# Optimization experiments

Measured on AMD Instinct MI355X. Metric: run time of the kernel, lower is better.

## Reference

```python
import jax, jax.numpy as jnp
import numpy as np

ALPHA = 0.15
KSIZE = 5
EPS = 1e-6


def _minmax_norm(x):
    # x: [B,1,H,W]; per-sample min-max normalize, 0.5 if nearly constant
    mn = x.min(axis=(1, 2, 3), keepdims=True)
    mx = x.max(axis=(1, 2, 3), keepdims=True)
    denom = mx - mn
    safe = jnp.where(denom > EPS, denom, 1.0)
    return jnp.where(denom > EPS, (x - mn) / safe, 0.5)


def _saliency_map(images, out_hw):
    # grayscale via luma weights
    w = jnp.array([0.299, 0.587, 0.114], dtype=images.dtype).reshape(1, 3, 1, 1)
    gray = (images * w).sum(axis=1, keepdims=True)  # [B,1,H,W]
    kernel = jnp.ones((1, 1, KSIZE, KSIZE), dtype=gray.dtype) / (KSIZE * KSIZE)
    dn = ('NCHW', 'OIHW', 'NCHW')
    local_mean = jax.lax.conv_general_dilated(gray, kernel, (1, 1), 'SAME', dimension_numbers=dn)
    local_mean_sq = jax.lax.conv_general_dilated(gray ** 2, kernel, (1, 1), 'SAME', dimension_numbers=dn)
    local_var = jnp.maximum(local_mean_sq - local_mean ** 2, 0.0)
    sal = _minmax_norm(local_var)
    if sal.shape[-2:] != out_hw:
        sal = jax.image.resize(sal, (sal.shape[0], 1, out_hw[0], out_hw[1]), method='bilinear')
    return jax.lax.stop_gradient(sal)  # computed under no_grad / detached in torch


def setup_inputs() -> dict:
    key = jax.random.key(0)
    k1, k2 = jax.random.split(key)
    features = jax.random.normal(k1, (64, 512, 28, 28), dtype=jnp.float32)
    images = jax.random.uniform(k2, (64, 3, 224, 224), dtype=jnp.float32)
    return {"features": features, "images": images}


def reference(features, images):
    sal = _saliency_map(images, features.shape[-2:])  # [B,1,Hf,Wf]
    attn = jnp.sqrt((features ** 2).mean(axis=1, keepdims=True))  # [B,1,Hf,Wf]
    attn = _minmax_norm(attn)
    loss = jnp.mean((attn - sal) ** 2)
    return ALPHA * loss
```

## Files before the change

### kernel.cpp

```cpp
#include <hip/hip_runtime.h>
#include <math.h>

#define BATCH 64
#define HIMG 224
#define WIMG 224
#define IMGPLANE (HIMG*WIMG)
#define CF 512
#define HF 28
#define WF 28
#define POS (HF*WF)
#define ALPHA_C 0.15f
#define EPS_C 1e-6f

#define STRIPS 14
#define SROWS 16
#define GROWS 20
#define GCOLS 228
#define GSTR 229
#define VSTR 261

#define NATTN 512
#define NVARH (STRIPS*BATCH)

#define OFF_HRES 0
#define HRES_CNT (BATCH*HIMG*WF)
#define OFF_BMM (OFF_HRES + HRES_CNT)
#define OFF_AP  (OFF_BMM + BATCH*STRIPS*2)
#define OFF_ACC (OFF_AP + 2*BATCH*POS)
#define OFF_CNT (OFF_ACC + 1)

__global__ __launch_bounds__(256) void fat_k(const float* __restrict__ img,
                                             const float* __restrict__ f,
                                             float* __restrict__ ws) {
    __shared__ float g[GROWS * GSTR];
    __shared__ float v[SROWS * VSTR];
    __shared__ float wred[8];
    int bid = blockIdx.x;
    int tid = threadIdx.x;

    if (bid < NATTN) {
        if (bid == 0 && tid == 0) {
            ws[OFF_ACC] = 0.0f;
            ((unsigned*)ws)[OFF_CNT] = 0u;
        }
        int p = (bid & 3) * 256 + tid;
        int b = (bid >> 2) & 63, z = bid >> 8;
        if (p >= POS) return;
        const float* fp = f + ((size_t)b * CF + (size_t)z * 256) * POS + p;
        float acc = 0.0f;
        #pragma unroll 16
        for (int c = 0; c < 256; c++) {
            float u = fp[(size_t)c * POS];
            acc += u * u;
        }
        ws[OFF_AP + ((size_t)z * BATCH + b) * POS + p] = acc;
        return;
    }

    int vb = bid - NATTN;
    int b = vb / STRIPS, sy = vb - b * STRIPS;
    int y0 = sy * SROWS;
    const float* imb = img + (size_t)b * 3 * IMGPLANE;

    for (int i = tid; i < GROWS * GCOLS; i += 256) {
        int gr = i / GCOLS, gc = i - gr * GCOLS;
        int gy = y0 - 2 + gr, gx = gc - 2;
        float u = 0.0f;
        if ((unsigned)gy < HIMG && (unsigned)gx < WIMG) {
            int o = gy * WIMG + gx;
            u = 0.299f * imb[o] + 0.587f * imb[IMGPLANE + o] + 0.114f * imb[2 * IMGPLANE + o];
        }
        g[gr * GSTR + gc] = u;
    }
    if (tid < SROWS * 8) {
        int r = tid >> 3, p = tid & 7;
        int jh = p + ((p < 4) ? 0 : 224);
        v[r * VSTR + jh + (jh >> 3)] = 0.0f;
    }
    __syncthreads();

    int r = tid >> 4, s = tid & 15;
    int x0 = 14 * s;
    const float* gr0 = g + r * GSTR;
    float c1[5], c2[5];
    #pragma unroll
    for (int m = 0; m < 5; m++) {
        float a = 0.0f, a2 = 0.0f;
        #pragma unroll
        for (int k = 0; k < 5; k++) {
            float u = gr0[k * GSTR + x0 + m];
            a += u; a2 += u * u;
        }
        c1[m] = a; c2[m] = a2;
    }
    float vmn = INFINITY, vmx = 0.0f;
    #pragma unroll
    for (int xi = 0; xi < 14; xi++) {
        int p = xi % 5;
        float s1 = c1[p], s2 = c2[p];
        #pragma unroll
        for (int m = 1; m < 5; m++) {
            s1 += c1[(p + m) % 5];
            s2 += c2[(p + m) % 5];
        }
        float m1 = s1 * 0.04f, m2 = s2 * 0.04f;
        float vv = fmaxf(m2 - m1 * m1, 0.0f);
        int jh = x0 + xi + 4;
        v[r * VSTR + jh + (jh >> 3)] = vv;
        vmn = fminf(vmn, vv); vmx = fmaxf(vmx, vv);
        if (xi < 13) {
            float a = 0.0f, a2 = 0.0f;
            #pragma unroll
            for (int k = 0; k < 5; k++) {
                float u = gr0[k * GSTR + x0 + xi + 5];
                a += u; a2 += u * u;
            }
            c1[p] = a; c2[p] = a2;
        }
    }
    #pragma unroll
    for (int o = 32; o > 0; o >>= 1) {
        vmn = fminf(vmn, __shfl_xor(vmn, o));
        vmx = fmaxf(vmx, __shfl_xor(vmx, o));
    }
    int w = tid >> 6;
    if ((tid & 63) == 0) { wred[w] = vmn; wred[4 + w] = vmx; }
    __syncthreads();
    if (tid == 0) {
        float mn = fminf(fminf(wred[0], wred[1]), fminf(wred[2], wred[3]));
        float mx = fmaxf(fmaxf(wred[4], wred[5]), fmaxf(wred[6], wred[7]));
        int blk = b * STRIPS + sy;
        ws[OFF_BMM + 2 * blk]     = mn;
        ws[OFF_BMM + 2 * blk + 1] = mx;
    }

    float* hb = ws + OFF_HRES + ((size_t)b * HIMG + y0) * WF;
    for (int idx = tid; idx < SROWS * WF; idx += 256) {
        int rr = idx / WF, i = idx - rr * WF;
        float acc = 0.0f, wsum = 0.0f;
        int j0 = 8 * i - 4;
        #pragma unroll
        for (int t = 0; t < 16; t++) {
            int j = j0 + t;
            float w_ = 8.0f - fabsf((float)t - 7.5f);
            int jh = j + 4;
            acc += w_ * v[rr * VSTR + jh + (jh >> 3)];
            if ((unsigned)j < WIMG) wsum += w_;
        }
        hb[idx] = acc / wsum;
    }
}

__global__ __launch_bounds__(256) void fused_k(float* __restrict__ ws,
                                               float* __restrict__ out) {
    __shared__ float hres[HIMG][WF + 1];
    __shared__ float wred[4];
    __shared__ float s_mn, s_mx;
    int b = blockIdx.x;
    int tid = threadIdx.x;

    if (tid < 64) {
        float mn = INFINITY, mx = 0.0f;
        if (tid < STRIPS) {
            mn = ws[OFF_BMM + 2 * (b * STRIPS + tid)];
            mx = ws[OFF_BMM + 2 * (b * STRIPS + tid) + 1];
        }
        #pragma unroll
        for (int o = 8; o > 0; o >>= 1) {
            mn = fminf(mn, __shfl_down(mn, o));
            mx = fmaxf(mx, __shfl_down(mx, o));
        }
        if (tid == 0) { s_mn = mn; s_mx = mx; }
    }

    const float* hg = ws + OFF_HRES + (size_t)b * HIMG * WF;
    for (int i = tid; i < HIMG * WF; i += 256) {
        int y = i / WF, x = i - y * WF;
        hres[y][x] = hg[i];
    }
    __syncthreads();

    float vmn = s_mn, vmx = s_mx;
    float vden = vmx - vmn;
    bool vok = vden > EPS_C;

    const float* a0 = ws + OFF_AP + (size_t)b * POS;
    const float* a1 = ws + OFF_AP + ((size_t)BATCH + b) * POS;
    float salv[4], attnv[4];
    float amn = INFINITY, amx = -INFINITY;
    #pragma unroll
    for (int k = 0; k < 4; k++) {
        int idx = tid + 256 * k;
        salv[k] = 0.0f; attnv[k] = 0.0f;
        if (idx < POS) {
            int yo = idx / WF, x = idx - yo * WF;
            float acc = 0.0f, wsum = 0.0f;
            int j0 = 8 * yo - 4;
            #pragma unroll
            for (int t = 0; t < 16; t++) {
                int j = j0 + t;
                float w = 8.0f - fabsf((float)t - 7.5f);
                if ((unsigned)j < HIMG) { acc += w * hres[j][x]; wsum += w; }
            }
            float sraw = acc / wsum;
            salv[k] = vok ? (sraw - vmn) / vden : 0.5f;
            float a = sqrtf((a0[idx] + a1[idx]) * (1.0f / CF));
            attnv[k] = a;
            amn = fminf(amn, a); amx = fmaxf(amx, a);
        }
    }

    #pragma unroll
    for (int o = 32; o > 0; o >>= 1) {
        amn = fminf(amn, __shfl_xor(amn, o));
        amx = fmaxf(amx, __shfl_xor(amx, o));
    }
    int w = tid >> 6;
    if ((tid & 63) == 0) wred[w] = amn;
    __syncthreads();
    if (tid == 0) s_mn = fminf(fminf(wred[0], wred[1]), fminf(wred[2], wred[3]));
    __syncthreads();
    if ((tid & 63) == 0) wred[w] = amx;
    __syncthreads();
    if (tid == 0) s_mx = fmaxf(fmaxf(wred[0], wred[1]), fmaxf(wred[2], wred[3]));
    __syncthreads();
    amn = s_mn; amx = s_mx;
    float aden = amx - amn;
    bool aok = aden > EPS_C;

    float lsum = 0.0f;
    #pragma unroll
    for (int k = 0; k < 4; k++) {
        int idx = tid + 256 * k;
        if (idx < POS) {
            float an = aok ? (attnv[k] - amn) / aden : 0.5f;
            float d = an - salv[k];
            lsum += d * d;
        }
    }
    #pragma unroll
    for (int o = 32; o > 0; o >>= 1) lsum += __shfl_xor(lsum, o);
    if ((tid & 63) == 0) wred[w] = lsum;
    __syncthreads();

    if (tid == 0) {
        float part = wred[0] + wred[1] + wred[2] + wred[3];
        atomicAdd(ws + OFF_ACC, part);
        __threadfence();
        unsigned old = atomicAdd((unsigned*)ws + OFF_CNT, 1u);
        if (old == BATCH - 1) {
            float tot = atomicAdd(ws + OFF_ACC, 0.0f);
            out[0] = tot * (ALPHA_C / (float)(BATCH * POS));
        }
    }
}

extern "C" void kernel_launch(void* const* d_in, const int* in_sizes, int n_in,
                              void* d_out, int out_size, void* d_ws, size_t ws_size,
                              hipStream_t stream) {
    const float* features = (const float*)d_in[0];
    const float* images   = (const float*)d_in[1];
    float* ws  = (float*)d_ws;
    float* out = (float*)d_out;

    hipLaunchKernelGGL(fat_k,   dim3(NATTN + NVARH), dim3(256), 0, stream,
                       images, features, ws);
    hipLaunchKernelGGL(fused_k, dim3(BATCH),         dim3(256), 0, stream, ws, out);
}
```

Measured before the change: 195.7 us.

## Vectorize feature and image loads, split channels 8-way, interleave block roles

```diff
diff --git a/kernel.cpp b/kernel.cpp
--- a/kernel.cpp
+++ b/kernel.cpp
@@ -18,6 +18,7 @@
 #define GCOLS 228
 #define GSTR 229
 #define VSTR 261
+#define SHN 4580
 
 #define NATTN 512
 #define NVARH (STRIPS*BATCH)
@@ -26,63 +27,71 @@
 #define HRES_CNT (BATCH*HIMG*WF)
 #define OFF_BMM (OFF_HRES + HRES_CNT)
 #define OFF_AP  (OFF_BMM + BATCH*STRIPS*2)
-#define OFF_ACC (OFF_AP + 2*BATCH*POS)
+#define OFF_ACC (OFF_AP + 8*BATCH*POS)
 #define OFF_CNT (OFF_ACC + 1)
 
 __global__ __launch_bounds__(256) void fat_k(const float* __restrict__ img,
                                              const float* __restrict__ f,
                                              float* __restrict__ ws) {
-    __shared__ float g[GROWS * GSTR];
-    __shared__ float v[SROWS * VSTR];
+    __shared__ float sh[SHN];
     __shared__ float wred[8];
     int bid = blockIdx.x;
     int tid = threadIdx.x;
-
-    if (bid < NATTN) {
-        if (bid == 0 && tid == 0) {
+    int g11 = bid / 11, r11 = bid - 11 * g11;
+
+    if (r11 < 4) {
+        int ab = g11 * 4 + r11;
+        if (ab == 0 && tid == 0) {
             ws[OFF_ACC] = 0.0f;
             ((unsigned*)ws)[OFF_CNT] = 0u;
         }
-        int p = (bid & 3) * 256 + tid;
-        int b = (bid >> 2) & 63, z = bid >> 8;
-        if (p >= POS) return;
-        const float* fp = f + ((size_t)b * CF + (size_t)z * 256) * POS + p;
-        float acc = 0.0f;
-        #pragma unroll 16
-        for (int c = 0; c < 256; c++) {
-            float u = fp[(size_t)c * POS];
-            acc += u * u;
-        }
-        ws[OFF_AP + ((size_t)z * BATCH + b) * POS + p] = acc;
+        if (tid >= 196) return;
+        int b = ab >> 3, z = ab & 7;
+        const float* fp = f + (size_t)(b * CF + z * 64) * POS + 4 * tid;
+        float ax = 0.0f, ay = 0.0f, az = 0.0f, aw = 0.0f;
+        #pragma unroll 8
+        for (int c = 0; c < 64; c++) {
+            float4 u = *(const float4*)(fp + (size_t)c * POS);
+            ax += u.x * u.x; ay += u.y * u.y; az += u.z * u.z; aw += u.w * u.w;
+        }
+        float4 o = make_float4(ax, ay, az, aw);
+        *(float4*)(ws + OFF_AP + (size_t)(z * BATCH + b) * POS + 4 * tid) = o;
         return;
     }
 
-    int vb = bid - NATTN;
+    int vb = g11 * 7 + (r11 - 4);
     int b = vb / STRIPS, sy = vb - b * STRIPS;
     int y0 = sy * SROWS;
     const float* imb = img + (size_t)b * 3 * IMGPLANE;
 
-    for (int i = tid; i < GROWS * GCOLS; i += 256) {
-        int gr = i / GCOLS, gc = i - gr * GCOLS;
-        int gy = y0 - 2 + gr, gx = gc - 2;
-        float u = 0.0f;
-        if ((unsigned)gy < HIMG && (unsigned)gx < WIMG) {
-            int o = gy * WIMG + gx;
-            u = 0.299f * imb[o] + 0.587f * imb[IMGPLANE + o] + 0.114f * imb[2 * IMGPLANE + o];
-        }
-        g[gr * GSTR + gc] = u;
-    }
-    if (tid < SROWS * 8) {
-        int r = tid >> 3, p = tid & 7;
-        int jh = p + ((p < 4) ? 0 : 224);
-        v[r * VSTR + jh + (jh >> 3)] = 0.0f;
+    for (int i = tid; i < GROWS * 56; i += 256) {
+        int gr = i / 56, q = i - gr * 56;
+        int gy = y0 - 2 + gr;
+        float gx0 = 0.0f, gx1 = 0.0f, gx2 = 0.0f, gx3 = 0.0f;
+        if ((unsigned)gy < HIMG) {
+            const float* row = imb + gy * WIMG + 4 * q;
+            float4 a = *(const float4*)(row);
+            float4 bb = *(const float4*)(row + IMGPLANE);
+            float4 c = *(const float4*)(row + 2 * IMGPLANE);
+            gx0 = 0.299f * a.x + 0.587f * bb.x + 0.114f * c.x;
+            gx1 = 0.299f * a.y + 0.587f * bb.y + 0.114f * c.y;
+            gx2 = 0.299f * a.z + 0.587f * bb.z + 0.114f * c.z;
+            gx3 = 0.299f * a.w + 0.587f * bb.w + 0.114f * c.w;
+        }
+        int base = gr * GSTR + 2 + 4 * q;
+        sh[base] = gx0; sh[base + 1] = gx1; sh[base + 2] = gx2; sh[base + 3] = gx3;
+    }
+    if (tid < GROWS * 4) {
+        int gr = tid >> 2, p = tid & 3;
+        int gc = (p < 2) ? p : (224 + p);
+        sh[gr * GSTR + gc] = 0.0f;
     }
     __syncthreads();
 
     int r = tid >> 4, s = tid & 15;
     int x0 = 14 * s;
-    const float* gr0 = g + r * GSTR;
-    float c1[5], c2[5];
+    const float* gr0 = sh + r * GSTR;
+    float c1[5], c2[5], vreg[14];
     #pragma unroll
     for (int m = 0; m < 5; m++) {
         float a = 0.0f, a2 = 0.0f;
@@ -105,8 +114,7 @@
         }
         float m1 = s1 * 0.04f, m2 = s2 * 0.04f;
         float vv = fmaxf(m2 - m1 * m1, 0.0f);
-        int jh = x0 + xi + 4;
-        v[r * VSTR + jh + (jh >> 3)] = vv;
+        vreg[xi] = vv;
         vmn = fminf(vmn, vv); vmx = fmaxf(vmx, vv);
         if (xi < 13) {
             float a = 0.0f, a2 = 0.0f;
@@ -123,8 +131,19 @@
         vmn = fminf(vmn, __shfl_xor(vmn, o));
         vmx = fmaxf(vmx, __shfl_xor(vmx, o));
     }
+    __syncthreads();
     int w = tid >> 6;
     if ((tid & 63) == 0) { wred[w] = vmn; wred[4 + w] = vmx; }
+    if (tid < SROWS * 8) {
+        int rr = tid >> 3, p = tid & 7;
+        int jh = p + ((p < 4) ? 0 : 224);
+        sh[rr * VSTR + jh + (jh >> 3)] = 0.0f;
+    }
+    #pragma unroll
+    for (int xi = 0; xi < 14; xi++) {
+        int jh = x0 + xi + 4;
+        sh[r * VSTR + jh + (jh >> 3)] = vreg[xi];
+    }
     __syncthreads();
     if (tid == 0) {
         float mn = fminf(fminf(wred[0], wred[1]), fminf(wred[2], wred[3]));
@@ -144,7 +163,7 @@
             int j = j0 + t;
             float w_ = 8.0f - fabsf((float)t - 7.5f);
             int jh = j + 4;
-            acc += w_ * v[rr * VSTR + jh + (jh >> 3)];
+            acc += w_ * sh[rr * VSTR + jh + (jh >> 3)];
             if ((unsigned)j < WIMG) wsum += w_;
         }
         hb[idx] = acc / wsum;
@@ -184,8 +203,7 @@
     float vden = vmx - vmn;
     bool vok = vden > EPS_C;
 
-    const float* a0 = ws + OFF_AP + (size_t)b * POS;
-    const float* a1 = ws + OFF_AP + ((size_t)BATCH + b) * POS;
+    const float* ap = ws + OFF_AP + (size_t)b * POS;
     float salv[4], attnv[4];
     float amn = INFINITY, amx = -INFINITY;
     #pragma unroll
@@ -204,7 +222,11 @@
             }
             float sraw = acc / wsum;
             salv[k] = vok ? (sraw - vmn) / vden : 0.5f;
-            float a = sqrtf((a0[idx] + a1[idx]) * (1.0f / CF));
+            float ssum = 0.0f;
+            #pragma unroll
+            for (int z = 0; z < 8; z++)
+                ssum += ap[(size_t)z * BATCH * POS + idx];
+            float a = sqrtf(ssum * (1.0f / CF));
             attnv[k] = a;
             amn = fminf(amn, a); amx = fmaxf(amx, a);
         }
```

Measured after the change: 191.8 us. -2.0%, faster.
